# Optimization experiments

Hardware: AMD Instinct MI355X
Metric: run time of the kernel (lower is better)

The kernel has to match this reference:

```python
import jax, jax.numpy as jnp
import numpy as np

N = 100000      # nodes
E = 1600000     # edges (no self-loops by construction)
DIN, DH, DOUT = 128, 128, 64
EPS = 1e-8      # torch cosine_similarity eps
LN_EPS = 1e-5


def _segsum(v, idx, n=N):
    return jax.ops.segment_sum(v, idx, num_segments=n)


def att_coef(feats, row, col):
    """Edge-wise cosine-sim attention + degree norm + self-loop append (torch no_grad block).
    Returns fixed-shape (row2, col2, vals2) of length E+N; filtered edges get weight 0
    (equivalent to removal for all scatter_add / message-passing math)."""
    dot = jnp.einsum('ed,ed->e', feats[row], feats[col])            # [E]
    nrm = jnp.maximum(jnp.linalg.norm(feats, axis=1), EPS)          # [N]
    sims = dot / (nrm[row] * nrm[col])
    keep = sims >= 0.1                                              # row!=col guaranteed
    sims = jnp.where(keep, sims, 0.0)
    deg = _segsum(sims, row)
    dinv = jnp.where(deg > 0, deg ** -0.5, 0.0)                     # inf -> 0
    sims = dinv[row] * sims * dinv[col]
    deg_new = _segsum(keep.astype(feats.dtype), col) + 1.0          # [N], >= 1
    self_val = 1.0 / deg_new
    vals = jnp.where(keep, jnp.exp(sims), 0.0)                      # removed edges -> 0
    sl = jnp.arange(N)
    row2 = jnp.concatenate([row, sl])
    col2 = jnp.concatenate([col, sl])
    vals2 = jnp.concatenate([vals, jnp.exp(self_val)])
    return row2, col2, vals2


def gcn_conv(x, row, col, w, W, b):
    """PyG GCNConv (normalize=True, add_self_loops=False) with given edge_weight."""
    h = x @ W                                                        # [N, out]
    deg = _segsum(w, col)
    dinv = jnp.where(deg > 0, deg ** -0.5, 0.0)
    norm = dinv[row] * w * dinv[col]                                 # [E+N]
    out = _segsum(norm[:, None] * h[row], col)                       # scatter to targets
    return out + b


def layer_norm(x, g, b):
    mu = jnp.mean(x, axis=-1, keepdims=True)
    var = jnp.mean((x - mu) ** 2, axis=-1, keepdims=True)
    return (x - mu) * jax.lax.rsqrt(var + LN_EPS) * g + b


def setup_inputs() -> dict:
    key = jax.random.key(0)
    ks = jax.random.split(key, 6)
    x = jax.random.normal(ks[0], (N, DIN), jnp.float32)
    row = jax.random.randint(ks[1], (E,), 0, N)
    col = jax.random.randint(ks[2], (E,), 0, N)
    col = jnp.where(col == row, (col + 1) % N, col)                  # no self-loops
    s1 = float(np.sqrt(6.0 / (DIN + DH)))                            # glorot
    s2 = float(np.sqrt(6.0 / (DH + DOUT)))
    W1 = jax.random.uniform(ks[3], (DIN, DH), jnp.float32, -s1, s1)
    W2 = jax.random.uniform(ks[4], (DH, DOUT), jnp.float32, -s2, s2)
    return dict(x=x, row=row, col=col,
                W1=W1, b1=jnp.zeros((DH,), jnp.float32),
                ln_g=jnp.ones((DH,), jnp.float32), ln_b=jnp.zeros((DH,), jnp.float32),
                W2=W2, b2=jnp.zeros((DOUT,), jnp.float32))


def reference(x, row, col, W1, b1, ln_g, ln_b, W2, b2):
    # layer 1: att_coef (no_grad) -> GCNConv -> LayerNorm -> ReLU (dropout is eval no-op)
    r2, c2, v2 = att_coef(jax.lax.stop_gradient(x), row, col)
    h = gcn_conv(x, r2, c2, v2, W1, b1)
    h = jax.nn.relu(layer_norm(h, ln_g, ln_b))
    # layer 2: att_coef on updated features (original edge list), final conv + log_softmax
    r2, c2, v2 = att_coef(jax.lax.stop_gradient(h), row, col)
    out = gcn_conv(h, r2, c2, v2, W2, b2)
    return jax.nn.log_softmax(out, axis=-1)
```

## Files before the change

### kernel.cpp

```cpp
#include <hip/hip_runtime.h>
#include <math.h>

#define EPSF 1e-8f
#define LN_EPS 1e-5f
#define BL_MARGIN 0.002f

#define BKT_SH 9
#define CHUNK 4096
#define BCAP 10240
#define DCAP 16384

typedef unsigned int  u32;
typedef unsigned short u16;
typedef _Float16 h2_t __attribute__((ext_vector_type(2)));
typedef _Float16 half8_t __attribute__((ext_vector_type(8)));
typedef float f32x4_t __attribute__((ext_vector_type(4)));

static __device__ inline u32 pack_h2(float a, float b) {
    h2_t h; h.x = (_Float16)a; h.y = (_Float16)b;
    return __builtin_bit_cast(u32, h);
}
static __device__ inline float h2lo(u32 u) {
    return (float)__builtin_bit_cast(h2_t, u).x;
}
static __device__ inline float h2hi(u32 u) {
    return (float)__builtin_bit_cast(h2_t, u).y;
}

static __device__ inline f32x4_t mfma16(uint4 a, uint4 b, f32x4_t c) {
    return __builtin_amdgcn_mfma_f32_16x16x32_f16(
        __builtin_bit_cast(half8_t, a), __builtin_bit_cast(half8_t, b), c, 0, 0, 0);
}
static __device__ inline float sel4(f32x4_t a, int m) {
    return m == 0 ? a[0] : m == 1 ? a[1] : m == 2 ? a[2] : a[3];
}

__global__ __launch_bounds__(256) void cast_norm_k(const float* __restrict__ feat,
    u32* __restrict__ fhf, float* __restrict__ nrm, float* __restrict__ deg1, int n) {
    int wid  = (blockIdx.x * 256 + threadIdx.x) >> 6;
    int lane = threadIdx.x & 63;
    if (wid >= n) return;
    float2 v = *(const float2*)(feat + (size_t)wid * 128 + lane * 2);
    float s = v.x * v.x + v.y * v.y;
    #pragma unroll
    for (int off = 32; off; off >>= 1) s += __shfl_xor(s, off, 64);
    float nv = fmaxf(sqrtf(s), EPSF);
    float inv = 1.0f / nv;
    fhf[(size_t)wid * 64 + lane] = pack_h2(v.x * inv, v.y * inv);
    if (lane == 0) { nrm[wid] = nv; deg1[wid] = 0.0f; }
}


__global__ __launch_bounds__(256) void binfill_k(const int* __restrict__ row,
    const int* __restrict__ col, int* __restrict__ bcur,
    int2* __restrict__ ebuf, int ecnt) {
    __shared__ int lc[256], ls[256], cur[256], gbase[256];
    __shared__ int2 pairs[CHUNK];
    __shared__ int dstv[CHUNK];
    int t = threadIdx.x;
    int e0 = blockIdx.x * CHUNK;
    int m = min(CHUNK, ecnt - e0);
    lc[t] = 0; cur[t] = 0; __syncthreads();
    int myc[CHUNK / 256], myr[CHUNK / 256];
    #pragma unroll
    for (int i = 0; i < CHUNK / 256; ++i) {
        int idx = t + i * 256;
        if (idx < m) {
            myc[i] = col[e0 + idx];
            myr[i] = row[e0 + idx];
            atomicAdd(&lc[myc[i] >> BKT_SH], 1);
        }
    }
    __syncthreads();
    int v = lc[t];
    ls[t] = v; __syncthreads();
    for (int off = 1; off < 256; off <<= 1) {
        int a = (t >= off) ? ls[t - off] : 0;
        __syncthreads();
        ls[t] += a;
        __syncthreads();
    }
    int ex = ls[t] - v;
    __syncthreads();
    ls[t] = ex;
    if (v) gbase[t] = atomicAdd(&bcur[t], v);
    __syncthreads();
    #pragma unroll
    for (int i = 0; i < CHUNK / 256; ++i) {
        int idx = t + i * 256;
        if (idx < m) {
            int b = myc[i] >> BKT_SH;
            int s = ls[b] + atomicAdd(&cur[b], 1);
            pairs[s] = make_int2(myc[i], myr[i]);
            int pos = gbase[b] + (s - ls[b]);
            dstv[s]  = (pos < BCAP) ? (b * BCAP + pos) : -1;
        }
    }
    __syncthreads();
    for (int s = t; s < m; s += 256) {
        int d = dstv[s];
        if (d >= 0) ebuf[d] = pairs[s];
    }
}

__global__ __launch_bounds__(256) void bucket_csr_k(const int2* __restrict__ ebuf,
    const int* __restrict__ bcur, int* __restrict__ startAll,
    int* __restrict__ cntAll, int* __restrict__ rowAll, int* __restrict__ colAll,
    int n) {
    __shared__ int sc[256];
    __shared__ int cnt[512], lst[512], cur[512];
    __shared__ int rowbuf[DCAP];
    int b = blockIdx.x, t = threadIdx.x;
    int c0 = b << BKT_SH;
    int bc = min(bcur[t], BCAP);
    sc[t] = bc; __syncthreads();
    for (int off = 1; off < 256; off <<= 1) {
        int a = (t >= off) ? sc[t - off] : 0;
        __syncthreads();
        sc[t] += a;
        __syncthreads();
    }
    int m  = min(bcur[b], BCAP);
    int g0 = sc[b] - m;
    size_t ebase = (size_t)b * BCAP;
    cnt[t] = 0; cnt[t + 256] = 0; cur[t] = 0; cur[t + 256] = 0;
    __syncthreads();
    for (int i = t; i < m; i += 256)
        atomicAdd(&cnt[ebuf[ebase + i].x - c0], 1);
    __syncthreads();
    int v0 = cnt[t], v1 = cnt[t + 256];
    lst[t] = v0; lst[t + 256] = v1; __syncthreads();
    for (int off = 1; off < 256; off <<= 1) {
        int a0 = (t >= off) ? lst[t - off] : 0;
        int a1 = (t >= off) ? lst[256 + t - off] : 0;
        __syncthreads();
        lst[t] += a0; lst[t + 256] += a1;
        __syncthreads();
    }
    int h0 = lst[255];
    int e0x = lst[t] - v0;
    int e1x = lst[t + 256] - v1 + h0;
    __syncthreads();
    lst[t] = e0x; lst[t + 256] = e1x;
    __syncthreads();
    #pragma unroll
    for (int half = 0; half < 2; ++half) {
        int i = t + half * 256;
        int c = c0 + i;
        if (c < n) { startAll[c] = g0 + lst[i]; cntAll[c] = cnt[i]; }
    }
    for (int i = t; i < m; i += 256) {
        int2 p = ebuf[ebase + i];
        int ci = p.x - c0;
        int pos = lst[ci] + atomicAdd(&cur[ci], 1);
        rowbuf[pos] = p.y;
    }
    __syncthreads();
    for (int i = t; i < m; i += 256)
        rowAll[g0 + i] = rowbuf[i];
    __syncthreads();
    #pragma unroll
    for (int half = 0; half < 2; ++half) {
        int i = t + half * 256;
        int base = lst[i], cn = cnt[i], cc = c0 + i;
        for (int k2 = 0; k2 < cn; ++k2) rowbuf[base + k2] = cc;
    }
    __syncthreads();
    for (int i = t; i < m; i += 256)
        colAll[g0 + i] = rowbuf[i];
}

__global__ __launch_bounds__(256) void edge_dot_flat_k(const u32* __restrict__ fhf,
    const float* __restrict__ feat32, const int* __restrict__ rowAll,
    const int* __restrict__ colAll, const float* __restrict__ nrm,
    float* __restrict__ sims, float* __restrict__ deg1, int ecnt) {
    int wv   = (blockIdx.x * 256 + threadIdx.x) >> 6;
    int lane = threadIdx.x & 63;
    int e0 = wv * 32;
    if (e0 >= ecnt) return;
    int lr = lane & 15, kq = lane >> 4;
    bool diag = (kq == (lr >> 2));
    int m3 = lane & 3;
    int em1 = ecnt - 1;

    int e1 = e0 + lr, e2 = e0 + 16 + lr;
    int e1c = min(e1, em1), e2c = min(e2, em1);
    int r1 = rowAll[e1c], c1 = colAll[e1c];
    int r2 = rowAll[e2c], c2 = colAll[e2c];
    const u32* pa1 = fhf + (size_t)c1 * 64 + kq * 4;
    const u32* pb1 = fhf + (size_t)r1 * 64 + kq * 4;
    const u32* pa2 = fhf + (size_t)c2 * 64 + kq * 4;
    const u32* pb2 = fhf + (size_t)r2 * 64 + kq * 4;
    uint4 a10 = *(const uint4*)(pa1);
    uint4 a11 = *(const uint4*)(pa1 + 16);
    uint4 a12 = *(const uint4*)(pa1 + 32);
    uint4 a13 = *(const uint4*)(pa1 + 48);
    uint4 b10 = *(const uint4*)(pb1);
    uint4 b11 = *(const uint4*)(pb1 + 16);
    uint4 b12 = *(const uint4*)(pb1 + 32);
    uint4 b13 = *(const uint4*)(pb1 + 48);
    uint4 a20 = *(const uint4*)(pa2);
    uint4 a21 = *(const uint4*)(pa2 + 16);
    uint4 a22 = *(const uint4*)(pa2 + 32);
    uint4 a23 = *(const uint4*)(pa2 + 48);
    uint4 b20 = *(const uint4*)(pb2);
    uint4 b21 = *(const uint4*)(pb2 + 16);
    uint4 b22 = *(const uint4*)(pb2 + 32);
    uint4 b23 = *(const uint4*)(pb2 + 48);

    f32x4_t acc1 = {0.f, 0.f, 0.f, 0.f};
    acc1 = mfma16(a10, b10, acc1);
    acc1 = mfma16(a11, b11, acc1);
    acc1 = mfma16(a12, b12, acc1);
    acc1 = mfma16(a13, b13, acc1);
    f32x4_t acc2 = {0.f, 0.f, 0.f, 0.f};
    acc2 = mfma16(a20, b20, acc2);
    acc2 = mfma16(a21, b21, acc2);
    acc2 = mfma16(a22, b22, acc2);
    acc2 = mfma16(a23, b23, acc2);

    float p1 = sel4(acc1, m3);
    float p2 = sel4(acc2, m3);
    bool act1 = diag && (e1 < ecnt);
    bool act2 = diag && (e2 < ecnt);

    unsigned long long bl = __ballot(act1 && fabsf(p1 - 0.1f) < BL_MARGIN);
    while (bl) {
        int src = __ffsll((unsigned long long)bl) - 1; bl &= bl - 1ull;
        int rt = __shfl(r1, src, 64);
        int ct = __shfl(c1, src, 64);
        float2 xa = *(const float2*)(feat32 + (size_t)rt * 128 + lane * 2);
        float2 xb = *(const float2*)(feat32 + (size_t)ct * 128 + lane * 2);
        float s2 = xa.x * xb.x + xa.y * xb.y;
        #pragma unroll
        for (int off = 32; off; off >>= 1) s2 += __shfl_xor(s2, off, 64);
        float pf = s2 / (nrm[rt] * nrm[ct]);
        if (lane == src) p1 = pf;
    }
    unsigned long long bl2 = __ballot(act2 && fabsf(p2 - 0.1f) < BL_MARGIN);
    while (bl2) {
        int src = __ffsll((unsigned long long)bl2) - 1; bl2 &= bl2 - 1ull;
        int rt = __shfl(r2, src, 64);
        int ct = __shfl(c2, src, 64);
        float2 xa = *(const float2*)(feat32 + (size_t)rt * 128 + lane * 2);
        float2 xb = *(const float2*)(feat32 + (size_t)ct * 128 + lane * 2);
        float s2 = xa.x * xb.x + xa.y * xb.y;
        #pragma unroll
        for (int off = 32; off; off >>= 1) s2 += __shfl_xor(s2, off, 64);
        float pf = s2 / (nrm[rt] * nrm[ct]);
        if (lane == src) p2 = pf;
    }
    if (act1) {
        float kv = (p1 >= 0.1f) ? p1 : 0.0f;
        sims[e1] = kv;
        if (kv > 0.0f) atomicAdd(&deg1[r1], kv);
    }
    if (act2) {
        float kv = (p2 >= 0.1f) ? p2 : 0.0f;
        sims[e2] = kv;
        if (kv > 0.0f) atomicAdd(&deg1[r2], kv);
    }
}

__global__ __launch_bounds__(256) void edge_c_csr_k(const float* __restrict__ sims,
    const int* __restrict__ rowAll, const int* __restrict__ startAll,
    const int* __restrict__ cntAll, const float* __restrict__ deg1,
    int2* __restrict__ kv, int* __restrict__ cntK, float* __restrict__ dinv2,
    float* __restrict__ cself, int n) {
    int wid  = (blockIdx.x * 256 + threadIdx.x) >> 6;
    int lane = threadIdx.x & 63;
    if (wid >= n) return;
    int s0 = startAll[wid], cnt = cntAll[wid];
    float degc = deg1[wid];
    float d1c = (degc > 0.0f) ? 1.0f / sqrtf(degc) : 0.0f;
    float vsum = 0.0f; int kc = 0;
    for (int jj = 0; jj < cnt; jj += 64) {
        int j = jj + lane;
        bool keep = false; int r = 0; float v = 0.0f;
        if (j < cnt) {
            float s = sims[s0 + j];
            if (s > 0.0f) {
                r = rowAll[s0 + j];
                float dr = 1.0f / sqrtf(deg1[r]);
                v = expf(dr * s * d1c);
                keep = true;
            }
        }
        unsigned long long m = __ballot(keep ? 1 : 0);
        if (keep) {
            int pre = __popcll(m & ((1ull << lane) - 1ull));
            int2 pk; pk.x = r; pk.y = __float_as_int(v);
            kv[s0 + kc + pre] = pk;
            vsum += v;
        }
        kc += __popcll(m);
    }
    #pragma unroll
    for (int off = 32; off; off >>= 1) vsum += __shfl_xor(vsum, off, 64);
    if (lane == 0) {
        float ws_ = expf(1.0f / ((float)kc + 1.0f));
        float dg = ws_ + vsum;
        float di = 1.0f / sqrtf(dg);
        dinv2[wid] = di;
        cself[wid] = di * ws_;
        cntK[wid]  = kc;
    }
}


__global__ __launch_bounds__(256) void gemm128_k(const float* __restrict__ A,
    const float* __restrict__ W, const float* __restrict__ scale,
    float* __restrict__ out, int n) {
    __shared__ float Ws[128 * 64];
    int colBase = blockIdx.y * 64;
    for (int i = threadIdx.x; i < 128 * 64 / 4; i += 256) {
        int k = i >> 4, c4 = i & 15;
        ((float4*)Ws)[i] = *(const float4*)(W + k * 128 + colBase + c4 * 4);
    }
    __syncthreads();
    const int TPN = 16;
    int group = threadIdx.x / TPN;
    int tin   = threadIdx.x % TPN;
    int nid   = (blockIdx.x * 16 + group) * 4;
    if (nid >= n) return;
    int dbase = tin * 4;
    int nm1 = n - 1;
    const float4* a0 = (const float4*)(A + (size_t)min(nid,     nm1) * 128);
    const float4* a1 = (const float4*)(A + (size_t)min(nid + 1, nm1) * 128);
    const float4* a2 = (const float4*)(A + (size_t)min(nid + 2, nm1) * 128);
    const float4* a3 = (const float4*)(A + (size_t)min(nid + 3, nm1) * 128);
    float4 acc0 = {0,0,0,0}, acc1 = {0,0,0,0}, acc2 = {0,0,0,0}, acc3 = {0,0,0,0};
    #pragma unroll 2
    for (int k4 = 0; k4 < 32; ++k4) {
        const float* wr = Ws + (k4 * 4) * 64 + dbase;
        float4 w0 = *(const float4*)(wr);
        float4 w1 = *(const float4*)(wr + 64);
        float4 w2 = *(const float4*)(wr + 128);
        float4 w3 = *(const float4*)(wr + 192);
        float4 v0 = a0[k4], v1 = a1[k4], v2 = a2[k4], v3 = a3[k4];
        acc0.x += v0.x*w0.x + v0.y*w1.x + v0.z*w2.x + v0.w*w3.x;
        acc0.y += v0.x*w0.y + v0.y*w1.y + v0.z*w2.y + v0.w*w3.y;
        acc0.z += v0.x*w0.z + v0.y*w1.z + v0.z*w2.z + v0.w*w3.z;
        acc0.w += v0.x*w0.w + v0.y*w1.w + v0.z*w2.w + v0.w*w3.w;
        acc1.x += v1.x*w0.x + v1.y*w1.x + v1.z*w2.x + v1.w*w3.x;
        acc1.y += v1.x*w0.y + v1.y*w1.y + v1.z*w2.y + v1.w*w3.y;
        acc1.z += v1.x*w0.z + v1.y*w1.z + v1.z*w2.z + v1.w*w3.z;
        acc1.w += v1.x*w0.w + v1.y*w1.w + v1.z*w2.w + v1.w*w3.w;
        acc2.x += v2.x*w0.x + v2.y*w1.x + v2.z*w2.x + v2.w*w3.x;
        acc2.y += v2.x*w0.y + v2.y*w1.y + v2.z*w2.y + v2.w*w3.y;
        acc2.z += v2.x*w0.z + v2.y*w1.z + v2.z*w2.z + v2.w*w3.z;
        acc2.w += v2.x*w0.w + v2.y*w1.w + v2.z*w2.w + v2.w*w3.w;
        acc3.x += v3.x*w0.x + v3.y*w1.x + v3.z*w2.x + v3.w*w3.x;
        acc3.y += v3.x*w0.y + v3.y*w1.y + v3.z*w2.y + v3.w*w3.y;
        acc3.z += v3.x*w0.z + v3.y*w1.z + v3.z*w2.z + v3.w*w3.z;
        acc3.w += v3.x*w0.w + v3.y*w1.w + v3.z*w2.w + v3.w*w3.w;
    }
    float4 accs[4] = {acc0, acc1, acc2, acc3};
    #pragma unroll
    for (int i = 0; i < 4; ++i) {
        if (nid + i < n) {
            float sc = scale[nid + i];
            float4 r; r.x = accs[i].x * sc; r.y = accs[i].y * sc;
            r.z = accs[i].z * sc; r.w = accs[i].w * sc;
            *(float4*)(out + (size_t)(nid + i) * 128 + colBase + dbase) = r;
        }
    }
}

__global__ __launch_bounds__(256) void gemm64_hf_k(const float* __restrict__ A,
    const float* __restrict__ W, const float* __restrict__ scale,
    u32* __restrict__ outhf, int n) {
    __shared__ float Ws[128 * 32];
    int colBase = blockIdx.y * 32;
    for (int i = threadIdx.x; i < 128 * 32 / 4; i += 256) {
        int k = i >> 3, c4 = i & 7;
        ((float4*)Ws)[i] = *(const float4*)(W + k * 64 + colBase + c4 * 4);
    }
    __syncthreads();
    const int TPN = 8;
    int group = threadIdx.x / TPN;
    int tin   = threadIdx.x % TPN;
    int nid   = (blockIdx.x * 32 + group) * 4;
    if (nid >= n) return;
    int dbase = tin * 4;
    int nm1 = n - 1;
    const float4* a0 = (const float4*)(A + (size_t)min(nid,     nm1) * 128);
    const float4* a1 = (const float4*)(A + (size_t)min(nid + 1, nm1) * 128);
    const float4* a2 = (const float4*)(A + (size_t)min(nid + 2, nm1) * 128);
    const float4* a3 = (const float4*)(A + (size_t)min(nid + 3, nm1) * 128);
    float4 acc0 = {0,0,0,0}, acc1 = {0,0,0,0}, acc2 = {0,0,0,0}, acc3 = {0,0,0,0};
    #pragma unroll 2
    for (int k4 = 0; k4 < 32; ++k4) {
        const float* wr = Ws + (k4 * 4) * 32 + dbase;
        float4 w0 = *(const float4*)(wr);
        float4 w1 = *(const float4*)(wr + 32);
        float4 w2 = *(const float4*)(wr + 64);
        float4 w3 = *(const float4*)(wr + 96);
        float4 v0 = a0[k4], v1 = a1[k4], v2 = a2[k4], v3 = a3[k4];
        acc0.x += v0.x*w0.x + v0.y*w1.x + v0.z*w2.x + v0.w*w3.x;
        acc0.y += v0.x*w0.y + v0.y*w1.y + v0.z*w2.y + v0.w*w3.y;
        acc0.z += v0.x*w0.z + v0.y*w1.z + v0.z*w2.z + v0.w*w3.z;
        acc0.w += v0.x*w0.w + v0.y*w1.w + v0.z*w2.w + v0.w*w3.w;
        acc1.x += v1.x*w0.x + v1.y*w1.x + v1.z*w2.x + v1.w*w3.x;
        acc1.y += v1.x*w0.y + v1.y*w1.y + v1.z*w2.y + v1.w*w3.y;
        acc1.z += v1.x*w0.z + v1.y*w1.z + v1.z*w2.z + v1.w*w3.z;
        acc1.w += v1.x*w0.w + v1.y*w1.w + v1.z*w2.w + v1.w*w3.w;
        acc2.x += v2.x*w0.x + v2.y*w1.x + v2.z*w2.x + v2.w*w3.x;
        acc2.y += v2.x*w0.y + v2.y*w1.y + v2.z*w2.y + v2.w*w3.y;
        acc2.z += v2.x*w0.z + v2.y*w1.z + v2.z*w2.z + v2.w*w3.z;
        acc2.w += v2.x*w0.w + v2.y*w1.w + v2.z*w2.w + v2.w*w3.w;
        acc3.x += v3.x*w0.x + v3.y*w1.x + v3.z*w2.x + v3.w*w3.x;
        acc3.y += v3.x*w0.y + v3.y*w1.y + v3.z*w2.y + v3.w*w3.y;
        acc3.z += v3.x*w0.z + v3.y*w1.z + v3.z*w2.z + v3.w*w3.z;
        acc3.w += v3.x*w0.w + v3.y*w1.w + v3.z*w2.w + v3.w*w3.w;
    }
    float4 accs[4] = {acc0, acc1, acc2, acc3};
    #pragma unroll
    for (int i = 0; i < 4; ++i) {
        if (nid + i < n) {
            float sc = scale[nid + i];
            u32 o0 = pack_h2(accs[i].x * sc, accs[i].y * sc);
            u32 o1 = pack_h2(accs[i].z * sc, accs[i].w * sc);
            *(uint2*)(outhf + (size_t)(nid + i) * 32 + (colBase >> 1) + tin * 2)
                = make_uint2(o0, o1);
        }
    }
}


__global__ __launch_bounds__(256) void gather_ln_k(const float* __restrict__ hs,
    const int2* __restrict__ kv, const int* __restrict__ startAll,
    const int* __restrict__ cntK, const float* __restrict__ dinv2,
    const float* __restrict__ cself, const float* __restrict__ bias,
    const float* __restrict__ g, const float* __restrict__ bln,
    float* __restrict__ outbuf, u32* __restrict__ outhf,
    float* __restrict__ nrm, float* __restrict__ deg1, int n) {
    int wid = (blockIdx.x * 256 + threadIdx.x) >> 5;
    int l   = threadIdx.x & 31;
    if (wid >= n) return;
    int s0 = startAll[wid], k = cntK[wid];
    if (l == 0) deg1[wid] = 0.0f;
    float4 acc = {0,0,0,0};
    int km1 = s0 + k - 1;
    for (int j0 = 0; j0 < k; j0 += 8) {
        int2 p[8];
        #pragma unroll
        for (int i = 0; i < 8; ++i) p[i] = kv[min(s0 + j0 + i, km1)];
        float4 h[8];
        #pragma unroll
        for (int i = 0; i < 8; ++i)
            h[i] = *(const float4*)(hs + (size_t)p[i].x * 128 + l * 4);
        #pragma unroll
        for (int i = 0; i < 8; ++i) {
            float v = (j0 + i < k) ? __int_as_float(p[i].y) : 0.0f;
            acc.x += v * h[i].x; acc.y += v * h[i].y;
            acc.z += v * h[i].z; acc.w += v * h[i].w;
        }
    }
    float di = dinv2[wid], cs = cself[wid];
    float4 hsv = *(const float4*)(hs + (size_t)wid * 128 + l * 4);
    float4 vb  = *(const float4*)(bias + l * 4);
    float x0 = di*acc.x + cs*hsv.x + vb.x;
    float x1 = di*acc.y + cs*hsv.y + vb.y;
    float x2 = di*acc.z + cs*hsv.z + vb.z;
    float x3 = di*acc.w + cs*hsv.w + vb.w;
    float s = x0 + x1 + x2 + x3;
    #pragma unroll
    for (int off = 16; off; off >>= 1) s += __shfl_xor(s, off, 64);
    float mu = s * (1.0f / 128.0f);
    float d0 = x0 - mu, d1 = x1 - mu, d2 = x2 - mu, d3 = x3 - mu;
    float vv = d0*d0 + d1*d1 + d2*d2 + d3*d3;
    #pragma unroll
    for (int off = 16; off; off >>= 1) vv += __shfl_xor(vv, off, 64);
    float rstd = 1.0f / sqrtf(vv * (1.0f / 128.0f) + LN_EPS);
    float4 vg  = *(const float4*)(g + l * 4);
    float4 vbl = *(const float4*)(bln + l * 4);
    float y0 = fmaxf(d0 * rstd * vg.x + vbl.x, 0.0f);
    float y1 = fmaxf(d1 * rstd * vg.y + vbl.y, 0.0f);
    float y2 = fmaxf(d2 * rstd * vg.z + vbl.z, 0.0f);
    float y3 = fmaxf(d3 * rstd * vg.w + vbl.w, 0.0f);
    float4 yo; yo.x = y0; yo.y = y1; yo.z = y2; yo.w = y3;
    *(float4*)(outbuf + (size_t)wid * 128 + l * 4) = yo;
    float ns = y0*y0 + y1*y1 + y2*y2 + y3*y3;
    #pragma unroll
    for (int off = 16; off; off >>= 1) ns += __shfl_xor(ns, off, 64);
    float nv = fmaxf(sqrtf(ns), EPSF);
    float inv = 1.0f / nv;
    uint2 oh; oh.x = pack_h2(y0 * inv, y1 * inv); oh.y = pack_h2(y2 * inv, y3 * inv);
    *(uint2*)(outhf + (size_t)wid * 64 + l * 2) = oh;
    if (l == 0) nrm[wid] = nv;
}

__global__ __launch_bounds__(256) void gather_lsm_hf_k(const u32* __restrict__ g2s,
    const int2* __restrict__ kv, const int* __restrict__ startAll,
    const int* __restrict__ cntK, const float* __restrict__ dinv2,
    const float* __restrict__ cself, const float* __restrict__ b2,
    float* __restrict__ out, int n) {
    int wid = (blockIdx.x * 256 + threadIdx.x) >> 5;
    int l   = threadIdx.x & 31;
    if (wid >= n) return;
    int s0 = startAll[wid], k = cntK[wid];
    float acc0 = 0.f, acc1 = 0.f;
    int km1 = s0 + k - 1;
    for (int j0 = 0; j0 < k; j0 += 8) {
        int2 p[8];
        #pragma unroll
        for (int i = 0; i < 8; ++i) p[i] = kv[min(s0 + j0 + i, km1)];
        u32 gv[8];
        #pragma unroll
        for (int i = 0; i < 8; ++i) gv[i] = g2s[(size_t)p[i].x * 32 + l];
        #pragma unroll
        for (int i = 0; i < 8; ++i) {
            float v = (j0 + i < k) ? __int_as_float(p[i].y) : 0.0f;
            acc0 += v * h2lo(gv[i]); acc1 += v * h2hi(gv[i]);
        }
    }
    float di = dinv2[wid], cs = cself[wid];
    u32 gsu = g2s[(size_t)wid * 32 + l];
    float2 vb = *(const float2*)(b2 + l * 2);
    float v0 = di * acc0 + cs * h2lo(gsu) + vb.x;
    float v1 = di * acc1 + cs * h2hi(gsu) + vb.y;
    float m = fmaxf(v0, v1);
    #pragma unroll
    for (int off = 16; off; off >>= 1) m = fmaxf(m, __shfl_xor(m, off, 64));
    float e = expf(v0 - m) + expf(v1 - m);
    #pragma unroll
    for (int off = 16; off; off >>= 1) e += __shfl_xor(e, off, 64);
    float lse = m + logf(e);
    *(float2*)(out + (size_t)wid * 64 + l * 2) = make_float2(v0 - lse, v1 - lse);
}


extern "C" void kernel_launch(void* const* d_in, const int* in_sizes, int n_in,
                              void* d_out, int out_size, void* d_ws, size_t ws_size,
                              hipStream_t stream) {
    (void)n_in; (void)out_size; (void)ws_size;
    const float* x   = (const float*)d_in[0];
    const int*   row = (const int*)d_in[1];
    const int*   col = (const int*)d_in[2];
    const float* W1  = (const float*)d_in[3];
    const float* b1  = (const float*)d_in[4];
    const float* lng = (const float*)d_in[5];
    const float* lnb = (const float*)d_in[6];
    const float* W2  = (const float*)d_in[7];
    const float* b2  = (const float*)d_in[8];
    float* out = (float*)d_out;

    const int N = in_sizes[0] / 128;
    const int E = in_sizes[1];

    int*   cntAll   = (int*)d_ws;
    int*   startAll = cntAll + N;
    int*   bcur     = startAll + N;
    float* nrm      = (float*)(bcur + 1024);
    float* deg1     = nrm + N;
    float* dinv2    = deg1 + N;
    float* cself    = dinv2 + N;
    int*   cntK     = (int*)(cself + N);
    int*   rowAll   = cntK + N;
    int*   colAll   = rowAll + E;
    int2*  kvp      = (int2*)(colAll + E);
    u32*   fhf      = (u32*)(kvp + E);
    u32*   g2shf    = fhf + (size_t)64 * N;
    float* big      = (float*)(g2shf + (size_t)32 * N);
    float* sims     = big;
    float* hs       = big;
    float* h2       = big + (size_t)128 * N;
    int2*  ebuf     = (int2*)big;

    const int waveBlocks  = (N + 3) / 4;
    const int halfBlocks  = (N + 7) / 8;
    const int flatBlocks  = (E + 127) / 128;
    const int NB          = (N + 511) >> 9;

    hipMemsetAsync(bcur, 0, 256 * sizeof(int), stream);
    binfill_k<<<(E + CHUNK - 1) / CHUNK, 256, 0, stream>>>(row, col, bcur, ebuf, E);
    bucket_csr_k<<<NB, 256, 0, stream>>>(ebuf, bcur, startAll, cntAll, rowAll,
                                         colAll, N);

    cast_norm_k<<<waveBlocks, 256, 0, stream>>>(x, fhf, nrm, deg1, N);
    edge_dot_flat_k<<<flatBlocks, 256, 0, stream>>>(fhf, x, rowAll, colAll, nrm,
                                                    sims, deg1, E);
    edge_c_csr_k<<<waveBlocks, 256, 0, stream>>>(sims, rowAll, startAll, cntAll, deg1,
                                                 kvp, cntK, dinv2, cself, N);
    gemm128_k<<<dim3((N + 63) / 64, 2), 256, 0, stream>>>(x, W1, dinv2, hs, N);
    gather_ln_k<<<halfBlocks, 256, 0, stream>>>(hs, kvp, startAll, cntK, dinv2, cself,
                                                b1, lng, lnb, h2, fhf, nrm, deg1, N);

    edge_dot_flat_k<<<flatBlocks, 256, 0, stream>>>(fhf, h2, rowAll, colAll, nrm,
                                                    sims, deg1, E);
    edge_c_csr_k<<<waveBlocks, 256, 0, stream>>>(sims, rowAll, startAll, cntAll, deg1,
                                                 kvp, cntK, dinv2, cself, N);
    gemm64_hf_k<<<dim3((N + 127) / 128, 2), 256, 0, stream>>>(h2, W2, dinv2, g2shf, N);
    gather_lsm_hf_k<<<halfBlocks, 256, 0, stream>>>(g2shf, kvp, startAll, cntK, dinv2,
                                                    cself, b2, out, N);
}
```

Measured before the change: 597.6 us.

## Use finer CSR buckets and full-width GEMM tiles reading A once

The CSR build now uses 512 buckets of 256 destination nodes with smaller chunks and bucket capacity. This gives more blocks in bucket_csr_k and less shared memory per block. Both GEMMs drop the 2-way column split in grid.y, so each block holds the whole weight matrix in LDS and reads each input row once. The cost is larger LDS use per block in gemm128 (64KB), which may reduce occupancy.

```diff
diff --git a/kernel.cpp b/kernel.cpp
--- a/kernel.cpp
+++ b/kernel.cpp
@@ -5,10 +5,10 @@
 #define LN_EPS 1e-5f
 #define BL_MARGIN 0.002f
 
-#define BKT_SH 9
-#define CHUNK 4096
-#define BCAP 10240
-#define DCAP 16384
+#define BKT_SH 8
+#define NBKT 512
+#define CHUNK 2048
+#define BCAP 5120
 
 typedef unsigned int  u32;
 typedef unsigned short u16;
@@ -54,13 +54,14 @@
 __global__ __launch_bounds__(256) void binfill_k(const int* __restrict__ row,
     const int* __restrict__ col, int* __restrict__ bcur,
     int2* __restrict__ ebuf, int ecnt) {
-    __shared__ int lc[256], ls[256], cur[256], gbase[256];
+    __shared__ int lc[NBKT], ls[NBKT], cur[NBKT], gbase[NBKT];
     __shared__ int2 pairs[CHUNK];
     __shared__ int dstv[CHUNK];
     int t = threadIdx.x;
     int e0 = blockIdx.x * CHUNK;
     int m = min(CHUNK, ecnt - e0);
-    lc[t] = 0; cur[t] = 0; __syncthreads();
+    lc[t] = 0; lc[t + 256] = 0; cur[t] = 0; cur[t + 256] = 0;
+    __syncthreads();
     int myc[CHUNK / 256], myr[CHUNK / 256];
     #pragma unroll
     for (int i = 0; i < CHUNK / 256; ++i) {
@@ -72,18 +73,22 @@
         }
     }
     __syncthreads();
-    int v = lc[t];
-    ls[t] = v; __syncthreads();
+    int v0 = lc[t], v1 = lc[t + 256];
+    ls[t] = v0; ls[t + 256] = v1; __syncthreads();
     for (int off = 1; off < 256; off <<= 1) {
-        int a = (t >= off) ? ls[t - off] : 0;
+        int a0 = (t >= off) ? ls[t - off] : 0;
+        int a1 = (t >= off) ? ls[256 + t - off] : 0;
         __syncthreads();
-        ls[t] += a;
+        ls[t] += a0; ls[t + 256] += a1;
         __syncthreads();
     }
-    int ex = ls[t] - v;
-    __syncthreads();
-    ls[t] = ex;
-    if (v) gbase[t] = atomicAdd(&bcur[t], v);
+    int h0 = ls[255];
+    int e0x = ls[t] - v0;
+    int e1x = ls[t + 256] - v1 + h0;
+    __syncthreads();
+    ls[t] = e0x; ls[t + 256] = e1x;
+    if (v0) gbase[t] = atomicAdd(&bcur[t], v0);
+    if (v1) gbase[t + 256] = atomicAdd(&bcur[t + 256], v1);
     __syncthreads();
     #pragma unroll
     for (int i = 0; i < CHUNK / 256; ++i) {
@@ -107,48 +112,42 @@
     const int* __restrict__ bcur, int* __restrict__ startAll,
     int* __restrict__ cntAll, int* __restrict__ rowAll, int* __restrict__ colAll,
     int n) {
-    __shared__ int sc[256];
-    __shared__ int cnt[512], lst[512], cur[512];
-    __shared__ int rowbuf[DCAP];
+    __shared__ int sc[NBKT];
+    __shared__ int cnt[256], lst[256], cur[256];
+    __shared__ int rowbuf[BCAP];
     int b = blockIdx.x, t = threadIdx.x;
     int c0 = b << BKT_SH;
-    int bc = min(bcur[t], BCAP);
-    sc[t] = bc; __syncthreads();
+    int s0v = min(bcur[t], BCAP), s1v = min(bcur[t + 256], BCAP);
+    sc[t] = s0v; sc[t + 256] = s1v; __syncthreads();
     for (int off = 1; off < 256; off <<= 1) {
-        int a = (t >= off) ? sc[t - off] : 0;
+        int a0 = (t >= off) ? sc[t - off] : 0;
+        int a1 = (t >= off) ? sc[256 + t - off] : 0;
         __syncthreads();
-        sc[t] += a;
+        sc[t] += a0; sc[t + 256] += a1;
         __syncthreads();
     }
     int m  = min(bcur[b], BCAP);
-    int g0 = sc[b] - m;
+    int g0 = ((b >= 256) ? sc[255] : 0) + sc[b] - m;
     size_t ebase = (size_t)b * BCAP;
-    cnt[t] = 0; cnt[t + 256] = 0; cur[t] = 0; cur[t + 256] = 0;
+    cnt[t] = 0; cur[t] = 0;
     __syncthreads();
     for (int i = t; i < m; i += 256)
         atomicAdd(&cnt[ebuf[ebase + i].x - c0], 1);
     __syncthreads();
-    int v0 = cnt[t], v1 = cnt[t + 256];
-    lst[t] = v0; lst[t + 256] = v1; __syncthreads();
+    int v = cnt[t];
+    lst[t] = v; __syncthreads();
     for (int off = 1; off < 256; off <<= 1) {
-        int a0 = (t >= off) ? lst[t - off] : 0;
-        int a1 = (t >= off) ? lst[256 + t - off] : 0;
+        int a = (t >= off) ? lst[t - off] : 0;
         __syncthreads();
-        lst[t] += a0; lst[t + 256] += a1;
+        lst[t] += a;
         __syncthreads();
     }
-    int h0 = lst[255];
-    int e0x = lst[t] - v0;
-    int e1x = lst[t + 256] - v1 + h0;
-    __syncthreads();
-    lst[t] = e0x; lst[t + 256] = e1x;
-    __syncthreads();
-    #pragma unroll
-    for (int half = 0; half < 2; ++half) {
-        int i = t + half * 256;
-        int c = c0 + i;
-        if (c < n) { startAll[c] = g0 + lst[i]; cntAll[c] = cnt[i]; }
-    }
+    int ex = lst[t] - v;
+    __syncthreads();
+    lst[t] = ex;
+    __syncthreads();
+    int c = c0 + t;
+    if (c < n) { startAll[c] = g0 + lst[t]; cntAll[c] = cnt[t]; }
     for (int i = t; i < m; i += 256) {
         int2 p = ebuf[ebase + i];
         int ci = p.x - c0;
@@ -159,10 +158,8 @@
     for (int i = t; i < m; i += 256)
         rowAll[g0 + i] = rowbuf[i];
     __syncthreads();
-    #pragma unroll
-    for (int half = 0; half < 2; ++half) {
-        int i = t + half * 256;
-        int base = lst[i], cn = cnt[i], cc = c0 + i;
+    {
+        int base = lst[t], cn = cnt[t], cc = c0 + t;
         for (int k2 = 0; k2 < cn; ++k2) rowbuf[base + k2] = cc;
     }
     __syncthreads();
@@ -311,12 +308,65 @@
 __global__ __launch_bounds__(256) void gemm128_k(const float* __restrict__ A,
     const float* __restrict__ W, const float* __restrict__ scale,
     float* __restrict__ out, int n) {
+    __shared__ float Ws[128 * 128];
+    for (int i = threadIdx.x; i < 128 * 128 / 4; i += 256)
+        ((float4*)Ws)[i] = ((const float4*)W)[i];
+    __syncthreads();
+    const int TPN = 32;
+    int group = threadIdx.x / TPN;
+    int tin   = threadIdx.x % TPN;
+    int nid   = (blockIdx.x * 8 + group) * 4;
+    if (nid >= n) return;
+    int dbase = tin * 4;
+    int nm1 = n - 1;
+    const float4* a0 = (const float4*)(A + (size_t)min(nid,     nm1) * 128);
+    const float4* a1 = (const float4*)(A + (size_t)min(nid + 1, nm1) * 128);
+    const float4* a2 = (const float4*)(A + (size_t)min(nid + 2, nm1) * 128);
+    const float4* a3 = (const float4*)(A + (size_t)min(nid + 3, nm1) * 128);
+    float4 acc0 = {0,0,0,0}, acc1 = {0,0,0,0}, acc2 = {0,0,0,0}, acc3 = {0,0,0,0};
+    #pragma unroll 2
+    for (int k4 = 0; k4 < 32; ++k4) {
+        const float* wr = Ws + (k4 * 4) * 128 + dbase;
+        float4 w0 = *(const float4*)(wr);
+        float4 w1 = *(const float4*)(wr + 128);
+        float4 w2 = *(const float4*)(wr + 256);
+        float4 w3 = *(const float4*)(wr + 384);
+        float4 v0 = a0[k4], v1 = a1[k4], v2 = a2[k4], v3 = a3[k4];
+        acc0.x += v0.x*w0.x + v0.y*w1.x + v0.z*w2.x + v0.w*w3.x;
+        acc0.y += v0.x*w0.y + v0.y*w1.y + v0.z*w2.y + v0.w*w3.y;
+        acc0.z += v0.x*w0.z + v0.y*w1.z + v0.z*w2.z + v0.w*w3.z;
+        acc0.w += v0.x*w0.w + v0.y*w1.w + v0.z*w2.w + v0.w*w3.w;
+        acc1.x += v1.x*w0.x + v1.y*w1.x + v1.z*w2.x + v1.w*w3.x;
+        acc1.y += v1.x*w0.y + v1.y*w1.y + v1.z*w2.y + v1.w*w3.y;
+        acc1.z += v1.x*w0.z + v1.y*w1.z + v1.z*w2.z + v1.w*w3.z;
+        acc1.w += v1.x*w0.w + v1.y*w1.w + v1.z*w2.w + v1.w*w3.w;
+        acc2.x += v2.x*w0.x + v2.y*w1.x + v2.z*w2.x + v2.w*w3.x;
+        acc2.y += v2.x*w0.y + v2.y*w1.y + v2.z*w2.y + v2.w*w3.y;
+        acc2.z += v2.x*w0.z + v2.y*w1.z + v2.z*w2.z + v2.w*w3.z;
+        acc2.w += v2.x*w0.w + v2.y*w1.w + v2.z*w2.w + v2.w*w3.w;
+        acc3.x += v3.x*w0.x + v3.y*w1.x + v3.z*w2.x + v3.w*w3.x;
+        acc3.y += v3.x*w0.y + v3.y*w1.y + v3.z*w2.y + v3.w*w3.y;
+        acc3.z += v3.x*w0.z + v3.y*w1.z + v3.z*w2.z + v3.w*w3.z;
+        acc3.w += v3.x*w0.w + v3.y*w1.w + v3.z*w2.w + v3.w*w3.w;
+    }
+    float4 accs[4] = {acc0, acc1, acc2, acc3};
+    #pragma unroll
+    for (int i = 0; i < 4; ++i) {
+        if (nid + i < n) {
+            float sc = scale[nid + i];
+            float4 r; r.x = accs[i].x * sc; r.y = accs[i].y * sc;
+            r.z = accs[i].z * sc; r.w = accs[i].w * sc;
+            *(float4*)(out + (size_t)(nid + i) * 128 + dbase) = r;
+        }
+    }
+}
+
+__global__ __launch_bounds__(256) void gemm64_hf_k(const float* __restrict__ A,
+    const float* __restrict__ W, const float* __restrict__ scale,
+    u32* __restrict__ outhf, int n) {
     __shared__ float Ws[128 * 64];
-    int colBase = blockIdx.y * 64;
-    for (int i = threadIdx.x; i < 128 * 64 / 4; i += 256) {
-        int k = i >> 4, c4 = i & 15;
-        ((float4*)Ws)[i] = *(const float4*)(W + k * 128 + colBase + c4 * 4);
-    }
+    for (int i = threadIdx.x; i < 128 * 64 / 4; i += 256)
+        ((float4*)Ws)[i] = ((const float4*)W)[i];
     __syncthreads();
     const int TPN = 16;
     int group = threadIdx.x / TPN;
@@ -360,68 +410,9 @@
     for (int i = 0; i < 4; ++i) {
         if (nid + i < n) {
             float sc = scale[nid + i];
-            float4 r; r.x = accs[i].x * sc; r.y = accs[i].y * sc;
-            r.z = accs[i].z * sc; r.w = accs[i].w * sc;
-            *(float4*)(out + (size_t)(nid + i) * 128 + colBase + dbase) = r;
-        }
-    }
-}
-
-__global__ __launch_bounds__(256) void gemm64_hf_k(const float* __restrict__ A,
-    const float* __restrict__ W, const float* __restrict__ scale,
-    u32* __restrict__ outhf, int n) {
-    __shared__ float Ws[128 * 32];
-    int colBase = blockIdx.y * 32;
-    for (int i = threadIdx.x; i < 128 * 32 / 4; i += 256) {
-        int k = i >> 3, c4 = i & 7;
-        ((float4*)Ws)[i] = *(const float4*)(W + k * 64 + colBase + c4 * 4);
-    }
-    __syncthreads();
-    const int TPN = 8;
-    int group = threadIdx.x / TPN;
-    int tin   = threadIdx.x % TPN;
-    int nid   = (blockIdx.x * 32 + group) * 4;
-    if (nid >= n) return;
-    int dbase = tin * 4;
-    int nm1 = n - 1;
-    const float4* a0 = (const float4*)(A + (size_t)min(nid,     nm1) * 128);
-    const float4* a1 = (const float4*)(A + (size_t)min(nid + 1, nm1) * 128);
-    const float4* a2 = (const float4*)(A + (size_t)min(nid + 2, nm1) * 128);
-    const float4* a3 = (const float4*)(A + (size_t)min(nid + 3, nm1) * 128);
-    float4 acc0 = {0,0,0,0}, acc1 = {0,0,0,0}, acc2 = {0,0,0,0}, acc3 = {0,0,0,0};
-    #pragma unroll 2
-    for (int k4 = 0; k4 < 32; ++k4) {
-        const float* wr = Ws + (k4 * 4) * 32 + dbase;
-        float4 w0 = *(const float4*)(wr);
-        float4 w1 = *(const float4*)(wr + 32);
-        float4 w2 = *(const float4*)(wr + 64);
-        float4 w3 = *(const float4*)(wr + 96);
-        float4 v0 = a0[k4], v1 = a1[k4], v2 = a2[k4], v3 = a3[k4];
-        acc0.x += v0.x*w0.x + v0.y*w1.x + v0.z*w2.x + v0.w*w3.x;
-        acc0.y += v0.x*w0.y + v0.y*w1.y + v0.z*w2.y + v0.w*w3.y;
-        acc0.z += v0.x*w0.z + v0.y*w1.z + v0.z*w2.z + v0.w*w3.z;
-        acc0.w += v0.x*w0.w + v0.y*w1.w + v0.z*w2.w + v0.w*w3.w;
-        acc1.x += v1.x*w0.x + v1.y*w1.x + v1.z*w2.x + v1.w*w3.x;
-        acc1.y += v1.x*w0.y + v1.y*w1.y + v1.z*w2.y + v1.w*w3.y;
-        acc1.z += v1.x*w0.z + v1.y*w1.z + v1.z*w2.z + v1.w*w3.z;
-        acc1.w += v1.x*w0.w + v1.y*w1.w + v1.z*w2.w + v1.w*w3.w;
-        acc2.x += v2.x*w0.x + v2.y*w1.x + v2.z*w2.x + v2.w*w3.x;
-        acc2.y += v2.x*w0.y + v2.y*w1.y + v2.z*w2.y + v2.w*w3.y;
-        acc2.z += v2.x*w0.z + v2.y*w1.z + v2.z*w2.z + v2.w*w3.z;
-        acc2.w += v2.x*w0.w + v2.y*w1.w + v2.z*w2.w + v2.w*w3.w;
-        acc3.x += v3.x*w0.x + v3.y*w1.x + v3.z*w2.x + v3.w*w3.x;
-        acc3.y += v3.x*w0.y + v3.y*w1.y + v3.z*w2.y + v3.w*w3.y;
-        acc3.z += v3.x*w0.z + v3.y*w1.z + v3.z*w2.z + v3.w*w3.z;
-        acc3.w += v3.x*w0.w + v3.y*w1.w + v3.z*w2.w + v3.w*w3.w;
-    }
-    float4 accs[4] = {acc0, acc1, acc2, acc3};
-    #pragma unroll
-    for (int i = 0; i < 4; ++i) {
-        if (nid + i < n) {
-            float sc = scale[nid + i];
             u32 o0 = pack_h2(accs[i].x * sc, accs[i].y * sc);
             u32 o1 = pack_h2(accs[i].z * sc, accs[i].w * sc);
-            *(uint2*)(outhf + (size_t)(nid + i) * 32 + (colBase >> 1) + tin * 2)
+            *(uint2*)(outhf + (size_t)(nid + i) * 32 + tin * 2)
                 = make_uint2(o0, o1);
         }
     }
@@ -571,9 +562,9 @@
     const int waveBlocks  = (N + 3) / 4;
     const int halfBlocks  = (N + 7) / 8;
     const int flatBlocks  = (E + 127) / 128;
-    const int NB          = (N + 511) >> 9;
-
-    hipMemsetAsync(bcur, 0, 256 * sizeof(int), stream);
+    const int NB          = (N + 255) >> 8;
+
+    hipMemsetAsync(bcur, 0, NBKT * sizeof(int), stream);
     binfill_k<<<(E + CHUNK - 1) / CHUNK, 256, 0, stream>>>(row, col, bcur, ebuf, E);
     bucket_csr_k<<<NB, 256, 0, stream>>>(ebuf, bcur, startAll, cntAll, rowAll,
                                          colAll, N);
@@ -583,7 +574,7 @@
                                                     sims, deg1, E);
     edge_c_csr_k<<<waveBlocks, 256, 0, stream>>>(sims, rowAll, startAll, cntAll, deg1,
                                                  kvp, cntK, dinv2, cself, N);
-    gemm128_k<<<dim3((N + 63) / 64, 2), 256, 0, stream>>>(x, W1, dinv2, hs, N);
+    gemm128_k<<<(N + 31) / 32, 256, 0, stream>>>(x, W1, dinv2, hs, N);
     gather_ln_k<<<halfBlocks, 256, 0, stream>>>(hs, kvp, startAll, cntK, dinv2, cself,
                                                 b1, lng, lnb, h2, fhf, nrm, deg1, N);
 
@@ -591,7 +582,7 @@
                                                     sims, deg1, E);
     edge_c_csr_k<<<waveBlocks, 256, 0, stream>>>(sims, rowAll, startAll, cntAll, deg1,
                                                  kvp, cntK, dinv2, cself, N);
-    gemm64_hf_k<<<dim3((N + 127) / 128, 2), 256, 0, stream>>>(h2, W2, dinv2, g2shf, N);
+    gemm64_hf_k<<<(N + 63) / 64, 256, 0, stream>>>(h2, W2, dinv2, g2shf, N);
     gather_lsm_hf_k<<<halfBlocks, 256, 0, stream>>>(g2shf, kvp, startAll, cntK, dinv2,
                                                     cself, b2, out, N);
 }
```

Result: no change. 603.3 us (+1.0%).
